# Performance work log

Measured on AMD Instinct MI355X. Metric: run time of the kernel, lower is better.

## Reference

```python
import jax, jax.numpy as jnp
import numpy as np

N = 16384
D = 128
TOPK = 32


def setup_inputs() -> dict:
    key = jax.random.key(0)
    kx, kw = jax.random.split(key)
    x = jax.random.normal(kx, (N,), dtype=jnp.float32)  # unused by the module's forward
    W = jax.random.normal(kw, (N, D), dtype=jnp.float32)  # embedding table (learned param)
    return {"x": x, "W": W}


def reference(x, W):
    # adj = E @ E^T : [N, N] similarity matrix
    adj = W @ W.T
    # per-row top-K (torch.topk along dim=1)
    vals, idx = jax.lax.top_k(adj, TOPK)  # [N, K] each
    # dense_to_sparse emits nonzeros in row-major order -> sort columns within each row.
    order = jnp.argsort(idx, axis=1)
    idx_s = jnp.take_along_axis(idx, order, axis=1)
    vals_s = jnp.take_along_axis(vals, order, axis=1)
    rows = jnp.repeat(jnp.arange(N, dtype=idx_s.dtype), TOPK)
    edge_index = jnp.stack([rows, idx_s.reshape(-1)])  # [2, N*K]
    edge_values = vals_s.reshape(-1)  # [N*K]
    return edge_index, edge_values
```

## Files before the change

### kernel.cpp

```cpp
#include <hip/hip_runtime.h>
#include <hip/hip_bf16.h>
#include <hip/hip_fp16.h>


#define N_ROWS 16384
#define DIM    128
#define TOPK   32
#define NK     (N_ROWS * TOPK)
#define ZTAU   2.45f
#define DELTA  0.05f
#define CAPL   192
#define WCAP   48
#define RPB    64
#define NWAVE  8
#define CPS    256
#define NSTG   (N_ROWS / CPS)
#define W1BIN  0.15625f
#define W2BIN  0.00244140625f

using short8   = __attribute__((ext_vector_type(8)))  short;
using floatx16 = __attribute__((ext_vector_type(16))) float;

__global__ __launch_bounds__(256)
void pack_kernel(const float* __restrict__ W, unsigned short* __restrict__ FA,
                 unsigned short* __restrict__ FB, float* __restrict__ norm) {
    const int wv = threadIdx.x >> 6, lane = threadIdx.x & 63;
    #pragma unroll
    for (int i = 0; i < 4; ++i) {
        const int row = blockIdx.x * 16 + wv * 4 + i;
        float2 v = *(const float2*)(W + (size_t)row * DIM + lane * 2);
        float ss = v.x * v.x + v.y * v.y;
        #pragma unroll
        for (int off = 32; off; off >>= 1) ss += __shfl_down(ss, off, 64);
        ss = __shfl(ss, 0, 64);
        const float nm = sqrtf(ss), inv = 1.0f / nm;
        __hip_bfloat16 b0 = __float2bfloat16(v.x), b1 = __float2bfloat16(v.y);
        const unsigned praw = (unsigned)(*(unsigned short*)&b0)
                            | ((unsigned)(*(unsigned short*)&b1) << 16);
        __hip_bfloat16 a0 = __float2bfloat16(v.x * inv), a1 = __float2bfloat16(v.y * inv);
        const unsigned pnrm = (unsigned)(*(unsigned short*)&a0)
                            | ((unsigned)(*(unsigned short*)&a1) << 16);
        const size_t dst = (size_t)(row >> 5) * 8192 + (size_t)(lane >> 2) * 512
                         + (size_t)(row & 31) * 16 + (size_t)(lane & 3) * 4;
        *(unsigned int*)((char*)FB + dst) = praw;
        *(unsigned int*)((char*)FA + dst) = pnrm;
        if (lane == 0) norm[row] = nm;
    }
}

__global__ __launch_bounds__(512, 2)
void fused_kernel(const unsigned short* __restrict__ FA,
                  const unsigned short* __restrict__ FB,
                  const float* __restrict__ W, const float* __restrict__ norm,
                  float* __restrict__ out) {
    __shared__ unsigned int scnt[RPB];
    __shared__ unsigned int candL[RPB * CAPL];
    __shared__ int          wcolS[NWAVE][WCAP];
    __shared__ double       dvalS[NWAVE][WCAP];
    __shared__ int          fcolS[NWAVE][TOPK];
    __shared__ float        fvalS[NWAVE][TOPK];
    __shared__ unsigned int wcntS[NWAVE], mcntS[NWAVE], fcntS[NWAVE];

    const int tid = threadIdx.x, lane = tid & 63, wid = tid >> 6;
    const int half = lane >> 5, l31 = lane & 31;
    const int rowbase = blockIdx.x * RPB;

    if (tid < RPB) scnt[tid] = 0u;
    __syncthreads();

    short8 afrag[2][8];
    #pragma unroll
    for (int mt = 0; mt < 2; ++mt) {
        const char* ab = (const char*)FA + (size_t)((rowbase >> 5) + mt) * 8192
                       + half * 512 + l31 * 16;
        #pragma unroll
        for (int kt = 0; kt < 8; ++kt) afrag[mt][kt] = *(const short8*)(ab + kt * 1024);
    }

    const int rbh = 4 * half;
    const char* bstream = (const char*)FB + (size_t)wid * 8192 + half * 512 + l31 * 16;

    auto step = [&](const short8* bfr, int s) {
        floatx16 acc0 = (floatx16)0.0f, acc1 = (floatx16)0.0f;
        #pragma unroll
        for (int kt = 0; kt < 8; ++kt) {
            acc0 = __builtin_amdgcn_mfma_f32_32x32x16_bf16(afrag[0][kt], bfr[kt], acc0, 0, 0, 0);
            acc1 = __builtin_amdgcn_mfma_f32_32x32x16_bf16(afrag[1][kt], bfr[kt], acc1, 0, 0, 0);
        }
        const unsigned pcol = (unsigned)(s * CPS + wid * 32 + l31) << 16;
        #pragma unroll
        for (int r = 0; r < 16; ++r) {
            if (acc0[r] > ZTAU) {
                const int rloc = rbh + (r & 3) + 8 * (r >> 2);
                unsigned slot = atomicAdd(&scnt[rloc], 1u);
                if (slot < CAPL)
                    candL[rloc * CAPL + slot] = pcol | __half_as_ushort(__float2half(acc0[r]));
            }
            if (acc1[r] > ZTAU) {
                const int rloc = 32 + rbh + (r & 3) + 8 * (r >> 2);
                unsigned slot = atomicAdd(&scnt[rloc], 1u);
                if (slot < CAPL)
                    candL[rloc * CAPL + slot] = pcol | __half_as_ushort(__float2half(acc1[r]));
            }
        }
    };

    short8 bX[8], bY[8];
    #pragma unroll
    for (int kt = 0; kt < 8; ++kt) bX[kt] = *(const short8*)(bstream + kt * 1024);
    for (int s = 0; s < NSTG; s += 2) {
        const char* p1 = bstream + (size_t)(s + 1) * 65536;
        #pragma unroll
        for (int kt = 0; kt < 8; ++kt) bY[kt] = *(const short8*)(p1 + kt * 1024);
        step(bX, s);
        if (s + 2 < NSTG) {
            const char* p2 = bstream + (size_t)(s + 2) * 65536;
            #pragma unroll
            for (int kt = 0; kt < 8; ++kt) bX[kt] = *(const short8*)(p2 + kt * 1024);
        }
        step(bY, s + 1);
    }
    __syncthreads();

    unsigned int* histW = (unsigned int*)&dvalS[wid][0];
    for (int rr = 0; rr < 8; ++rr) {
        const int rloc = wid * 8 + rr;
        const int rowg = rowbase + rloc;
        int n = (int)scnt[rloc]; if (n > CAPL) n = CAPL;
        const unsigned int* cl = &candL[rloc * CAPL];

        if (lane == 0) { wcntS[wid] = 0u; mcntS[wid] = 0u; fcntS[wid] = 0u; }
        histW[lane] = 0u;
        for (int i = lane; i < n; i += 64) {
            const float v = __half2float(__ushort_as_half((unsigned short)(cl[i] & 0xFFFFu)));
            int b = (int)((v - ZTAU) * (1.0f / W1BIN));
            b = b < 0 ? 0 : (b > 63 ? 63 : b);
            atomicAdd(&histW[b], 1u);
        }
        unsigned sfx = histW[lane];
        #pragma unroll
        for (int off = 1; off < 64; off <<= 1) {
            unsigned t = __shfl_down(sfx, off, 64);
            if (lane + off < 64) sfx += t;
        }
        unsigned long long mk = __ballot(sfx >= (unsigned)TOPK);
        const int b1 = mk ? (63 - __clzll(mk)) : 0;
        unsigned Gup = __shfl(sfx, (b1 + 1) & 63, 64);
        if (b1 == 63) Gup = 0u;
        const float lo1 = ZTAU + (float)b1 * W1BIN;

        histW[lane] = 0u;
        for (int i = lane; i < n; i += 64) {
            const float v = __half2float(__ushort_as_half((unsigned short)(cl[i] & 0xFFFFu)));
            if (v >= lo1 && v < lo1 + W1BIN) {
                int b = (int)((v - lo1) * (1.0f / W2BIN));
                b = b < 0 ? 0 : (b > 63 ? 63 : b);
                atomicAdd(&histW[b], 1u);
            }
        }
        unsigned sfx2 = histW[lane];
        #pragma unroll
        for (int off = 1; off < 64; off <<= 1) {
            unsigned t = __shfl_down(sfx2, off, 64);
            if (lane + off < 64) sfx2 += t;
        }
        sfx2 += Gup;
        mk = __ballot(sfx2 >= (unsigned)TOPK);
        const int b2 = mk ? (63 - __clzll(mk)) : 0;
        const float vlo = lo1 + (float)b2 * W2BIN;
        const float vhi = vlo + W2BIN;

        for (int i = lane; i < n; i += 64) {
            const unsigned e = cl[i];
            const float v = __half2float(__ushort_as_half((unsigned short)(e & 0xFFFFu)));
            if (v > vhi + DELTA) {
                atomicAdd(&mcntS[wid], 1u);
            } else if (v >= vlo - DELTA) {
                unsigned t = atomicAdd(&wcntS[wid], 1u);
                if (t < WCAP) wcolS[wid][t] = (int)(e >> 16);
            }
        }
        const int m = (int)mcntS[wid];
        int wn = (int)wcntS[wid]; if (wn > WCAP) wn = WCAP;
        int need = TOPK - m; if (need < 0) need = 0;

        if (lane < wn) {
            const int col = wcolS[wid][lane] & (N_ROWS - 1);
            const float4* wa = (const float4*)(W + (size_t)rowg * DIM);
            const float4* wb = (const float4*)(W + (size_t)col * DIM);
            double d0 = 0, d1 = 0, d2 = 0, d3 = 0;
            #pragma unroll
            for (int k = 0; k < DIM / 4; ++k) {
                const float4 x = wa[k]; const float4 y = wb[k];
                d0 += (double)x.x * y.x; d1 += (double)x.y * y.y;
                d2 += (double)x.z * y.z; d3 += (double)x.w * y.w;
            }
            dvalS[wid][lane] = (d0 + d1) + (d2 + d3);
        }
        if (lane < wn) {
            const double dv = dvalS[wid][lane]; const int c = wcolS[wid][lane];
            int r = 0;
            for (int u = 0; u < wn; ++u) {
                const double du = dvalS[wid][u];
                r += (du > dv || (du == dv && wcolS[wid][u] < c)) ? 1 : 0;
            }
            if (r < need) {
                unsigned slot = atomicAdd(&fcntS[wid], 1u);
                if (slot < TOPK) { fcolS[wid][slot] = c; fvalS[wid][slot] = (float)dv; }
            }
        }
        const float nm = norm[rowg];
        for (int i = lane; i < n; i += 64) {
            const unsigned e = cl[i];
            const float v = __half2float(__ushort_as_half((unsigned short)(e & 0xFFFFu)));
            if (v > vhi + DELTA) {
                unsigned slot = atomicAdd(&fcntS[wid], 1u);
                if (slot < TOPK) { fcolS[wid][slot] = (int)(e >> 16); fvalS[wid][slot] = v * nm; }
            }
        }
        int fn = (int)fcntS[wid]; if (fn > TOPK) fn = TOPK;
        if (lane < fn) {
            const int c = fcolS[wid][lane];
            int pos = 0;
            for (int j = 0; j < fn; ++j) pos += (fcolS[wid][j] < c) ? 1 : 0;
            const size_t base = (size_t)rowg * TOPK + pos;
            out[base]                  = (float)rowg;
            out[NK + base]             = (float)c;
            out[2 * (size_t)NK + base] = fvalS[wid][lane];
        }
    }
}

extern "C" void kernel_launch(void* const* d_in, const int* in_sizes, int n_in,
                              void* d_out, int out_size, void* d_ws, size_t ws_size,
                              hipStream_t stream) {
    (void)in_sizes; (void)n_in; (void)out_size; (void)ws_size;
    const float* W   = (const float*)d_in[1];
    float*       out = (float*)d_out;

    char* ws = (char*)d_ws;
    unsigned short* FA   = (unsigned short*)ws;
    unsigned short* FB   = (unsigned short*)(ws + (size_t)4194304);
    float*          norm = (float*)(ws + (size_t)8388608);

    pack_kernel<<<N_ROWS / 16, 256, 0, stream>>>(W, FA, FB, norm);
    fused_kernel<<<N_ROWS / RPB, 512, 0, stream>>>(FA, FB, W, norm, out);
}
```

Measured before the change: 233.9 us.

## Double waves per block to 16 and restage pack kernel through LDS

The fused kernel now launches 1024 threads (16 waves) per block instead of 512. Each wave streams a distinct slice of columns, so a stage covers 512 columns and the stage count halves. In the per-row selection phase each wave now handles 4 rows instead of 8. The pack kernel is rewritten to load 32 rows with coalesced float4 reads into LDS, compute norms with a shuffle reduction, and write the blocked bf16 layouts contiguously. The aim is more parallelism per block and better pack coalescing, at the cost of one resident block per CU and higher LDS use.

Result: slower. 433.0 us (+85.1%).

```diff
diff --git a/kernel.cpp b/kernel.cpp
--- a/kernel.cpp
+++ b/kernel.cpp
@@ -12,8 +12,8 @@
 #define CAPL   192
 #define WCAP   48
 #define RPB    64
-#define NWAVE  8
-#define CPS    256
+#define NWAVE  16
+#define CPS    512
 #define NSTG   (N_ROWS / CPS)
 #define W1BIN  0.15625f
 #define W2BIN  0.00244140625f
@@ -21,34 +21,48 @@
 using short8   = __attribute__((ext_vector_type(8)))  short;
 using floatx16 = __attribute__((ext_vector_type(16))) float;
 
+#define PK_ROWS 32
 __global__ __launch_bounds__(256)
 void pack_kernel(const float* __restrict__ W, unsigned short* __restrict__ FA,
                  unsigned short* __restrict__ FB, float* __restrict__ norm) {
-    const int wv = threadIdx.x >> 6, lane = threadIdx.x & 63;
+    __shared__ float lds[PK_ROWS * 132];
+    __shared__ float nrmS[PK_ROWS];
+    const int t  = threadIdx.x;
+    const int rb = blockIdx.x * PK_ROWS;
+
+    const float4* src = (const float4*)(W + (size_t)rb * DIM);
     #pragma unroll
     for (int i = 0; i < 4; ++i) {
-        const int row = blockIdx.x * 16 + wv * 4 + i;
-        float2 v = *(const float2*)(W + (size_t)row * DIM + lane * 2);
-        float ss = v.x * v.x + v.y * v.y;
-        #pragma unroll
-        for (int off = 32; off; off >>= 1) ss += __shfl_down(ss, off, 64);
-        ss = __shfl(ss, 0, 64);
-        const float nm = sqrtf(ss), inv = 1.0f / nm;
-        __hip_bfloat16 b0 = __float2bfloat16(v.x), b1 = __float2bfloat16(v.y);
-        const unsigned praw = (unsigned)(*(unsigned short*)&b0)
-                            | ((unsigned)(*(unsigned short*)&b1) << 16);
-        __hip_bfloat16 a0 = __float2bfloat16(v.x * inv), a1 = __float2bfloat16(v.y * inv);
-        const unsigned pnrm = (unsigned)(*(unsigned short*)&a0)
-                            | ((unsigned)(*(unsigned short*)&a1) << 16);
-        const size_t dst = (size_t)(row >> 5) * 8192 + (size_t)(lane >> 2) * 512
-                         + (size_t)(row & 31) * 16 + (size_t)(lane & 3) * 4;
-        *(unsigned int*)((char*)FB + dst) = praw;
-        *(unsigned int*)((char*)FA + dst) = pnrm;
-        if (lane == 0) norm[row] = nm;
-    }
+        const int f = t + 256 * i;
+        const float4 v = src[f];
+        const int r = f >> 5, j = f & 31;
+        *(float4*)&lds[r * 132 + j * 4] = v;
+        float ss = v.x * v.x + v.y * v.y + v.z * v.z + v.w * v.w;
+        #pragma unroll
+        for (int off = 1; off < 32; off <<= 1) ss += __shfl_xor(ss, off, 64);
+        if (j == 0) nrmS[r] = sqrtf(ss);
+    }
+    __syncthreads();
+
+    const size_t blkoff = (size_t)blockIdx.x * 8192;
+    unsigned* fa = (unsigned*)((char*)FA + blkoff);
+    unsigned* fb = (unsigned*)((char*)FB + blkoff);
+    #pragma unroll
+    for (int i = 0; i < 8; ++i) {
+        const int d   = t + 256 * i;
+        const int q   = d >> 7, r31 = (d >> 2) & 31, w = d & 3;
+        const float f0 = lds[r31 * 132 + q * 8 + w * 2];
+        const float f1 = lds[r31 * 132 + q * 8 + w * 2 + 1];
+        const float inv = 1.0f / nrmS[r31];
+        __hip_bfloat16 b0 = __float2bfloat16(f0), b1 = __float2bfloat16(f1);
+        fb[d] = (unsigned)(*(unsigned short*)&b0) | ((unsigned)(*(unsigned short*)&b1) << 16);
+        __hip_bfloat16 a0 = __float2bfloat16(f0 * inv), a1 = __float2bfloat16(f1 * inv);
+        fa[d] = (unsigned)(*(unsigned short*)&a0) | ((unsigned)(*(unsigned short*)&a1) << 16);
+    }
+    if (t < PK_ROWS) norm[rb + t] = nrmS[t];
 }
 
-__global__ __launch_bounds__(512, 2)
+__global__ __launch_bounds__(1024, 1)
 void fused_kernel(const unsigned short* __restrict__ FA,
                   const unsigned short* __restrict__ FB,
                   const float* __restrict__ W, const float* __restrict__ norm,
@@ -109,12 +123,12 @@
     #pragma unroll
     for (int kt = 0; kt < 8; ++kt) bX[kt] = *(const short8*)(bstream + kt * 1024);
     for (int s = 0; s < NSTG; s += 2) {
-        const char* p1 = bstream + (size_t)(s + 1) * 65536;
+        const char* p1 = bstream + (size_t)(s + 1) * 131072;
         #pragma unroll
         for (int kt = 0; kt < 8; ++kt) bY[kt] = *(const short8*)(p1 + kt * 1024);
         step(bX, s);
         if (s + 2 < NSTG) {
-            const char* p2 = bstream + (size_t)(s + 2) * 65536;
+            const char* p2 = bstream + (size_t)(s + 2) * 131072;
             #pragma unroll
             for (int kt = 0; kt < 8; ++kt) bX[kt] = *(const short8*)(p2 + kt * 1024);
         }
@@ -123,8 +137,8 @@
     __syncthreads();
 
     unsigned int* histW = (unsigned int*)&dvalS[wid][0];
-    for (int rr = 0; rr < 8; ++rr) {
-        const int rloc = wid * 8 + rr;
+    for (int rr = 0; rr < 4; ++rr) {
+        const int rloc = wid * 4 + rr;
         const int rowg = rowbase + rloc;
         int n = (int)scnt[rloc]; if (n > CAPL) n = CAPL;
         const unsigned int* cl = &candL[rloc * CAPL];
@@ -140,8 +154,8 @@
         unsigned sfx = histW[lane];
         #pragma unroll
         for (int off = 1; off < 64; off <<= 1) {
-            unsigned t = __shfl_down(sfx, off, 64);
-            if (lane + off < 64) sfx += t;
+            unsigned u = __shfl_down(sfx, off, 64);
+            if (lane + off < 64) sfx += u;
         }
         unsigned long long mk = __ballot(sfx >= (unsigned)TOPK);
         const int b1 = mk ? (63 - __clzll(mk)) : 0;
@@ -161,8 +175,8 @@
         unsigned sfx2 = histW[lane];
         #pragma unroll
         for (int off = 1; off < 64; off <<= 1) {
-            unsigned t = __shfl_down(sfx2, off, 64);
-            if (lane + off < 64) sfx2 += t;
+            unsigned u = __shfl_down(sfx2, off, 64);
+            if (lane + off < 64) sfx2 += u;
         }
         sfx2 += Gup;
         mk = __ballot(sfx2 >= (unsigned)TOPK);
@@ -176,8 +190,8 @@
             if (v > vhi + DELTA) {
                 atomicAdd(&mcntS[wid], 1u);
             } else if (v >= vlo - DELTA) {
-                unsigned t = atomicAdd(&wcntS[wid], 1u);
-                if (t < WCAP) wcolS[wid][t] = (int)(e >> 16);
+                unsigned u = atomicAdd(&wcntS[wid], 1u);
+                if (u < WCAP) wcolS[wid][u] = (int)(e >> 16);
             }
         }
         const int m = (int)mcntS[wid];
@@ -243,6 +257,6 @@
     unsigned short* FB   = (unsigned short*)(ws + (size_t)4194304);
     float*          norm = (float*)(ws + (size_t)8388608);
 
-    pack_kernel<<<N_ROWS / 16, 256, 0, stream>>>(W, FA, FB, norm);
-    fused_kernel<<<N_ROWS / RPB, 512, 0, stream>>>(FA, FB, W, norm, out);
+    pack_kernel<<<N_ROWS / PK_ROWS, 256, 0, stream>>>(W, FA, FB, norm);
+    fused_kernel<<<N_ROWS / RPB, 1024, 0, stream>>>(FA, FB, W, norm, out);
 }
```
